# Optimization experiments

Measured on AMD Instinct MI355X. Metric: run time of the kernel, lower is better.

Reference implementation:

```python
import jax, jax.numpy as jnp
import numpy as np
from jax import lax

DIM = 128
DEPTH = 2
OUT_DIM = 256
DIM_HEAD = 64
HEADS = 8
WS = 16
INNER = DIM_HEAD * HEADS
EPS = 1e-5
SCALE = DIM_HEAD ** (-0.5)


def setup_inputs() -> dict:
    key = jax.random.key(0)
    ks = jax.random.split(key, 20)
    s = 0.02
    L = DEPTH
    inp = {
        "x": jax.random.normal(ks[0], (1, DIM, 256, 256), dtype=jnp.float32),
        "ln1_g": jnp.ones((L, DIM), dtype=jnp.float32),
        "ln1_b": jnp.zeros((L, DIM), dtype=jnp.float32),
        "wq": jax.random.normal(ks[1], (L, INNER, DIM), dtype=jnp.float32) * s,
        "wkv": jax.random.normal(ks[2], (L, 2 * INNER, DIM), dtype=jnp.float32) * s,
        "wo": jax.random.normal(ks[3], (L, DIM, INNER), dtype=jnp.float32) * s,
        "bo": jnp.zeros((L, DIM), dtype=jnp.float32),
        "ln2_g": jnp.ones((L, DIM), dtype=jnp.float32),
        "ln2_b": jnp.zeros((L, DIM), dtype=jnp.float32),
        "w_in": jax.random.normal(ks[4], (L, DIM, DIM), dtype=jnp.float32) * s,
        "b_in": jnp.zeros((L, DIM), dtype=jnp.float32),
        "w_c3": jax.random.normal(ks[5], (L, OUT_DIM, DIM, 3, 3), dtype=jnp.float32) * s,
        "b_c3": jnp.zeros((L, OUT_DIM), dtype=jnp.float32),
        "w_c1": jax.random.normal(ks[6], (L, DIM, OUT_DIM), dtype=jnp.float32) * s,
        "b_c1": jnp.zeros((L, DIM), dtype=jnp.float32),
        "w_outer": jax.random.normal(ks[7], (DIM, DIM), dtype=jnp.float32) * s,
        "b_outer": jnp.zeros((DIM,), dtype=jnp.float32),
    }
    return inp


def _layernorm(x, g, b):
    # channel-wise (dim=1) norm; note torch code uses (std + eps), not sqrt(var + eps)
    mean = jnp.mean(x, axis=1, keepdims=True)
    std = jnp.sqrt(jnp.var(x, axis=1, keepdims=True))
    return (x - mean) / (std + EPS) * g[None, :, None, None] + b[None, :, None, None]


def _conv1x1(w, x, b=None):
    y = jnp.einsum('oi,bihw->bohw', w, x)
    if b is not None:
        y = y + b[None, :, None, None]
    return y


def _to_windows(t, B, H, W):
    # [B, HEADS*DIM_HEAD, H, W] -> [B*HEADS*nx*ny, WS*WS, DIM_HEAD]
    nx, ny = H // WS, W // WS
    t = t.reshape(B, HEADS, DIM_HEAD, nx, WS, ny, WS)
    t = t.transpose(0, 1, 3, 5, 4, 6, 2)
    return t.reshape(B * HEADS * nx * ny, WS * WS, DIM_HEAD)


def _from_windows(t, B, H, W):
    nx, ny = H // WS, W // WS
    t = t.reshape(B, HEADS, nx, ny, WS, WS, DIM_HEAD)
    t = t.transpose(0, 1, 6, 2, 4, 3, 5)
    return t.reshape(B, HEADS * DIM_HEAD, H, W)


def _attention(x, wq_l, wkv_l, wo_l, bo_l):
    B, _, H, W = x.shape
    q = _conv1x1(wq_l, x)
    kv = _conv1x1(wkv_l, x)
    k, v = kv[:, :INNER], kv[:, INNER:]
    q = _to_windows(q, B, H, W)
    k = _to_windows(k, B, H, W)
    v = _to_windows(v, B, H, W)
    sim = jnp.einsum('bid,bjd->bij', q, k) * SCALE  # [nwin, 256, 256]
    attn = jax.nn.softmax(sim, axis=-1)
    out = jnp.einsum('bij,bjd->bid', attn, v)
    out = _from_windows(out, B, H, W)
    return _conv1x1(wo_l, out, bo_l)


def _feedforward(x, w_in_l, b_in_l, w_c3_l, b_c3_l, w_c1_l, b_c1_l):
    h = _conv1x1(w_in_l, x, b_in_l)
    h = lax.conv_general_dilated(h, w_c3_l, window_strides=(1, 1), padding='SAME',
                                 dimension_numbers=('NCHW', 'OIHW', 'NCHW'))
    h = h + b_c3_l[None, :, None, None]
    h = jax.nn.gelu(h, approximate=False)
    return _conv1x1(w_c1_l, h, b_c1_l)


def reference(x, ln1_g, ln1_b, wq, wkv, wo, bo, ln2_g, ln2_b,
              w_in, b_in, w_c3, b_c3, w_c1, b_c1, w_outer, b_outer):
    for l in range(DEPTH):
        xn = _layernorm(x, ln1_g[l], ln1_b[l])
        x = _attention(xn, wq[l], wkv[l], wo[l], bo[l]) + x
        xn = _layernorm(x, ln2_g[l], ln2_b[l])
        x = _feedforward(xn, w_in[l], b_in[l], w_c3[l], b_c3[l], w_c1[l], b_c1[l]) + x
    return _conv1x1(w_outer, x, b_outer) + x
```

## Files before the change

kernel.cpp:

```cpp
#include <hip/hip_runtime.h>
#include <hip/hip_bf16.h>
#include <math.h>

typedef __hip_bfloat16 bf16;
typedef float f4 __attribute__((ext_vector_type(4)));
typedef short s8 __attribute__((ext_vector_type(8)));
typedef unsigned int u2 __attribute__((ext_vector_type(2)));
typedef unsigned int u4v __attribute__((ext_vector_type(4)));

__device__ __forceinline__ void gload16(const void* g, char* l) {
  __builtin_amdgcn_global_load_lds(
      (const __attribute__((address_space(1))) unsigned int*)g,
      (__attribute__((address_space(3))) unsigned int*)l, 16, 0, 0);
}
__device__ __forceinline__ unsigned short bfr(float f) {
  bf16 h = __float2bfloat16(f);
  return *(unsigned short*)&h;
}
__device__ __forceinline__ unsigned int pk2(float a, float b) {
  return (unsigned int)bfr(a) | ((unsigned int)bfr(b) << 16);
}
__device__ __forceinline__ unsigned int pkt(float a, float b) {
  return __builtin_amdgcn_perm(__float_as_uint(b), __float_as_uint(a), 0x07060302u);
}

__global__ __launch_bounds__(256) void prep_w(
    const float* __restrict__ wq, const float* __restrict__ wkv,
    const float* __restrict__ wo, const float* __restrict__ win,
    const float* __restrict__ wc3, const float* __restrict__ wc1,
    const float* __restrict__ wout, ushort* __restrict__ cw)
{
  int i = blockIdx.x * 256 + threadIdx.x;
  float v;
  if (i < 131072) v = wq[i];
  else if (i < 393216) v = wkv[i - 131072];
  else if (i < 524288) v = wo[i - 393216];
  else if (i < 557056) v = win[i - 524288];
  else if (i < 1146880) {
    int j = i - 557056; int lyr = j / 294912; int r = j - lyr * 294912;
    int m = r / 1152; int k = r - m * 1152; int tap = k >> 7; int ic = k & 127;
    v = wc3[(((size_t)lyr * 256 + m) * 128 + ic) * 9 + tap];
  }
  else if (i < 1212416) v = wc1[i - 1146880];
  else if (i < 1228800) v = wout[i - 1212416];
  else if (i < 1230848) { cw[i] = 0; return; }
  else return;
  cw[i] = bfr(v);
}

template<bool NCHW>
__global__ __launch_bounds__(256) void ln_nhwc(
    const float* __restrict__ x, const float* __restrict__ g,
    const float* __restrict__ b, ushort* __restrict__ y)
{
  const int p = blockIdx.x * 256 + threadIdx.x;
  f4 v[32];
  float s = 0.f, s2 = 0.f;
  if constexpr (NCHW) {
#pragma unroll
    for (int i = 0; i < 32; ++i)
#pragma unroll
      for (int j = 0; j < 4; ++j) {
        float t = x[(size_t)(i * 4 + j) * 65536 + p];
        v[i][j] = t; s += t; s2 += t * t;
      }
  } else {
    const f4* base = (const f4*)(x + (size_t)p * 128);
#pragma unroll
    for (int i = 0; i < 32; ++i) {
      v[i] = base[i];
#pragma unroll
      for (int j = 0; j < 4; ++j) { s += v[i][j]; s2 += v[i][j] * v[i][j]; }
    }
  }
  float mean = s * (1.f / 128.f);
  float var = s2 * (1.f / 128.f) - mean * mean;
  var = var > 0.f ? var : 0.f;
  float inv = 1.f / (sqrtf(var) + 1e-5f);
  u2* dst = (u2*)(y + (size_t)p * 128);
#pragma unroll
  for (int i = 0; i < 32; ++i) {
    f4 gg = *(const f4*)(g + i * 4);
    f4 bb = *(const f4*)(b + i * 4);
    float f0 = (v[i][0] - mean) * inv * gg[0] + bb[0];
    float f1 = (v[i][1] - mean) * inv * gg[1] + bb[1];
    float f2 = (v[i][2] - mean) * inv * gg[2] + bb[2];
    float f3 = (v[i][3] - mean) * inv * gg[3] + bb[3];
    u2 st; st.x = pk2(f0, f1); st.y = pk2(f2, f3);
    dst[i] = st;
  }
}

template<int MODE>
__global__ __launch_bounds__(256) void gemm_nhwc(
    const ushort* __restrict__ A, const ushort* __restrict__ X,
    const float* __restrict__ bias, const float* __restrict__ res,
    void* __restrict__ out, ushort* __restrict__ out2,
    const float* __restrict__ lng, const float* __restrict__ lnb,
    ushort* __restrict__ xn, const int K, const int M)
{
  __shared__ __align__(16) char sm[32768];
  const int tid = threadIdx.x, w = tid >> 6, l = tid & 63;
  const int quad = l >> 4, l15 = l & 15;
  const int n0 = blockIdx.x * 128, m0 = blockIdx.y * 128;
  const int mh = (w & 1) * 64, nh = (w >> 1) * 64;
  const f4 fz = {0.f, 0.f, 0.f, 0.f};
  f4 acc[4][4];
#pragma unroll
  for (int a = 0; a < 4; ++a)
#pragma unroll
    for (int b2 = 0; b2 < 4; ++b2) acc[a][b2] = fz;

  const int KI = K >> 6;
  for (int kk = 0; kk < KI; ++kk) {
    if (kk) __syncthreads();
    const int k0 = kk << 6;
#pragma unroll
    for (int j = 0; j < 4; ++j) {
      int p = j * 256 + tid, r = p >> 3, c = (p & 7) ^ (r & 7);
      gload16(A + (size_t)(m0 + r) * K + k0 + c * 8, sm + (j * 256 + w * 64) * 16);
    }
#pragma unroll
    for (int j = 0; j < 4; ++j) {
      int p = j * 256 + tid, r = p >> 3, c = (p & 7) ^ (r & 7);
      gload16(X + (size_t)(n0 + r) * K + k0 + c * 8, sm + 16384 + (j * 256 + w * 64) * 16);
    }
    __syncthreads();
#pragma unroll
    for (int ks = 0; ks < 2; ++ks) {
      s8 af[4], bx[4];
#pragma unroll
      for (int mt = 0; mt < 4; ++mt) {
        int rr = mh + mt * 16 + l15;
        af[mt] = *(const s8*)(sm + rr * 128 + (((ks * 4 + quad) ^ (rr & 7)) << 4));
      }
#pragma unroll
      for (int nt = 0; nt < 4; ++nt) {
        int rr = nh + nt * 16 + l15;
        bx[nt] = *(const s8*)(sm + 16384 + rr * 128 + (((ks * 4 + quad) ^ (rr & 7)) << 4));
      }
#pragma unroll
      for (int mt = 0; mt < 4; ++mt)
#pragma unroll
        for (int nt = 0; nt < 4; ++nt)
          acc[mt][nt] = __builtin_amdgcn_mfma_f32_16x16x32_bf16(af[mt], bx[nt], acc[mt][nt], 0, 0, 0);
    }
  }

  if constexpr (MODE == 5 || MODE == 6) {
    float s1[4] = {0.f, 0.f, 0.f, 0.f}, s2[4] = {0.f, 0.f, 0.f, 0.f};
#pragma unroll
    for (int mt = 0; mt < 4; ++mt) {
      const int m = mh + mt * 16 + quad * 4;
      f4 bb = *(const f4*)(bias + m);
#pragma unroll
      for (int nt = 0; nt < 4; ++nt) {
        const int n = n0 + nh + nt * 16 + l15;
        f4 v = acc[mt][nt] + bb;
        if constexpr (MODE == 5) {
          f4 r = *(const f4*)(res + (size_t)n * 128 + m);
          v += r;
        } else {
          f4 r;
#pragma unroll
          for (int i = 0; i < 4; ++i) r[i] = res[(size_t)(m + i) * 65536 + n];
          v += r;
        }
        *(f4*)((float*)out + (size_t)n * 128 + m) = v;
        acc[mt][nt] = v;
        s1[nt] += v[0] + v[1] + v[2] + v[3];
        s2[nt] += v[0] * v[0] + v[1] * v[1] + v[2] * v[2] + v[3] * v[3];
      }
    }
    __syncthreads();
    float* pb = (float*)sm;
#pragma unroll
    for (int nt = 0; nt < 4; ++nt) {
      float a1 = s1[nt], a2 = s2[nt];
      a1 += __shfl_xor(a1, 16, 64); a1 += __shfl_xor(a1, 32, 64);
      a2 += __shfl_xor(a2, 16, 64); a2 += __shfl_xor(a2, 32, 64);
      s1[nt] = a1; s2[nt] = a2;
      if (quad == 0) {
        int pn = nh + nt * 16 + l15;
        pb[((w & 1) * 128 + pn) * 2]     = a1;
        pb[((w & 1) * 128 + pn) * 2 + 1] = a2;
      }
    }
    __syncthreads();
#pragma unroll
    for (int nt = 0; nt < 4; ++nt) {
      int pn = nh + nt * 16 + l15;
      float t1 = s1[nt] + pb[((1 - (w & 1)) * 128 + pn) * 2];
      float t2 = s2[nt] + pb[((1 - (w & 1)) * 128 + pn) * 2 + 1];
      float mean = t1 * (1.f / 128.f);
      float var = t2 * (1.f / 128.f) - mean * mean;
      var = var > 0.f ? var : 0.f;
      s1[nt] = mean;
      s2[nt] = 1.f / (sqrtf(var) + 1e-5f);
    }
#pragma unroll
    for (int mt = 0; mt < 4; ++mt) {
      const int m = mh + mt * 16 + quad * 4;
      f4 gg = *(const f4*)(lng + m);
      f4 b2 = *(const f4*)(lnb + m);
#pragma unroll
      for (int nt = 0; nt < 4; ++nt) {
        const int n = n0 + nh + nt * 16 + l15;
        f4 v = acc[mt][nt];
        float mean = s1[nt], inv = s2[nt];
        float f0 = (v[0] - mean) * inv * gg[0] + b2[0];
        float f1 = (v[1] - mean) * inv * gg[1] + b2[1];
        float f2 = (v[2] - mean) * inv * gg[2] + b2[2];
        float f3 = (v[3] - mean) * inv * gg[3] + b2[3];
        u2 st; st.x = pk2(f0, f1); st.y = pk2(f2, f3);
        *(u2*)(xn + (size_t)n * 128 + m) = st;
      }
    }
    return;
  }

#pragma unroll
  for (int mt = 0; mt < 4; ++mt) {
#pragma unroll
    for (int nt = 0; nt < 4; ++nt) {
      const int m = m0 + mh + mt * 16 + quad * 4;
      const int n = n0 + nh + nt * 16 + l15;
      f4 bb = *(const f4*)(bias + m);
      f4 v = acc[mt][nt] + bb;
      if constexpr (MODE == 0) {
        u2 st; st.x = pk2(v[0], v[1]); st.y = pk2(v[2], v[3]);
        *(u2*)((ushort*)out + (size_t)n * M + m) = st;
      } else if constexpr (MODE == 1 || MODE == 3) {
        f4 r = *(const f4*)(res + (size_t)n * M + m);
        v += r;
        *(f4*)((float*)out + (size_t)n * M + m) = v;
        if constexpr (MODE == 3) {
          u2 st; st.x = pk2(v[0], v[1]); st.y = pk2(v[2], v[3]);
          *(u2*)(out2 + (size_t)n * M + m) = st;
        }
      } else if constexpr (MODE == 4) {
        f4 r;
#pragma unroll
        for (int i = 0; i < 4; ++i) r[i] = res[(size_t)(m + i) * 65536 + n];
        v += r;
        *(f4*)((float*)out + (size_t)n * M + m) = v;
      } else {
        f4 r = *(const f4*)(res + (size_t)n * M + m);
#pragma unroll
        for (int i = 0; i < 4; ++i)
          ((float*)out)[(size_t)(m + i) * 65536 + n] = v[i] + r[i];
      }
    }
  }
}

__global__ __launch_bounds__(256) void conv3_kernel(
    const ushort* __restrict__ A, const ushort* __restrict__ X,
    const float* __restrict__ bias, ushort* __restrict__ out,
    const ushort* __restrict__ zp)
{
  __shared__ __align__(16) char sm[32768];
  const int tid = threadIdx.x, w = tid >> 6, l = tid & 63;
  const int quad = l >> 4, l15 = l & 15;
  const int n0 = blockIdx.x * 128, m0 = blockIdx.y * 128;
  const int mh = (w & 1) * 64, nh = (w >> 1) * 64;
  const f4 fz = {0.f, 0.f, 0.f, 0.f};
  f4 acc[4][4];
#pragma unroll
  for (int a = 0; a < 4; ++a)
#pragma unroll
    for (int b2 = 0; b2 < 4; ++b2) acc[a][b2] = fz;

  for (int kk = 0; kk < 18; ++kk) {
    if (kk) __syncthreads();
    const int tap = kk >> 1, ky = tap / 3, kx = tap - ky * 3;
    const int dn = (ky - 1) * 256 + (kx - 1);
    const int kseg = (kk & 1) << 6;
#pragma unroll
    for (int j = 0; j < 4; ++j) {
      int p = j * 256 + tid, r = p >> 3, c = (p & 7) ^ (r & 7);
      gload16(A + (size_t)(m0 + r) * 1152 + kk * 64 + c * 8, sm + (j * 256 + w * 64) * 16);
    }
#pragma unroll
    for (int j = 0; j < 4; ++j) {
      int p = j * 256 + tid, r = p >> 3, c = (p & 7) ^ (r & 7);
      int nl = n0 + r;
      int ys = (nl >> 8) + ky - 1, xs = (nl & 255) + kx - 1;
      const ushort* gp = ((unsigned)ys < 256u && (unsigned)xs < 256u)
                         ? X + (size_t)(nl + dn) * 128 + kseg + c * 8 : zp;
      gload16(gp, sm + 16384 + (j * 256 + w * 64) * 16);
    }
    __syncthreads();
#pragma unroll
    for (int ks = 0; ks < 2; ++ks) {
      s8 af[4], bx[4];
#pragma unroll
      for (int mt = 0; mt < 4; ++mt) {
        int rr = mh + mt * 16 + l15;
        af[mt] = *(const s8*)(sm + rr * 128 + (((ks * 4 + quad) ^ (rr & 7)) << 4));
      }
#pragma unroll
      for (int nt = 0; nt < 4; ++nt) {
        int rr = nh + nt * 16 + l15;
        bx[nt] = *(const s8*)(sm + 16384 + rr * 128 + (((ks * 4 + quad) ^ (rr & 7)) << 4));
      }
#pragma unroll
      for (int mt = 0; mt < 4; ++mt)
#pragma unroll
        for (int nt = 0; nt < 4; ++nt)
          acc[mt][nt] = __builtin_amdgcn_mfma_f32_16x16x32_bf16(af[mt], bx[nt], acc[mt][nt], 0, 0, 0);
    }
  }
#pragma unroll
  for (int mt = 0; mt < 4; ++mt) {
#pragma unroll
    for (int nt = 0; nt < 4; ++nt) {
      const int m = m0 + mh + mt * 16 + quad * 4;
      const int n = n0 + nh + nt * 16 + l15;
      f4 bb = *(const f4*)(bias + m);
      f4 v = acc[mt][nt] + bb;
      float g0 = 0.5f * v[0] * (1.f + erff(v[0] * 0.70710678118f));
      float g1 = 0.5f * v[1] * (1.f + erff(v[1] * 0.70710678118f));
      float g2 = 0.5f * v[2] * (1.f + erff(v[2] * 0.70710678118f));
      float g3 = 0.5f * v[3] * (1.f + erff(v[3] * 0.70710678118f));
      u2 st; st.x = pk2(g0, g1); st.y = pk2(g2, g3);
      *(u2*)(out + (size_t)n * 256 + m) = st;
    }
  }
}

__global__ __launch_bounds__(512) void attn_kernel(
    const ushort* __restrict__ xn, const ushort* __restrict__ wq,
    const ushort* __restrict__ wkv, ushort* __restrict__ ao)
{
  __shared__ __align__(16) char sm[147456];
  const int tid = threadIdx.x, w = tid >> 6, l = tid & 63;
  const int quad = l >> 4, l15 = l & 15;
  const int win = blockIdx.x, head = blockIdx.y;
  const int nbase = ((win >> 4) << 12) + ((win & 15) << 4);
  char* RX  = sm;
  char* RW  = sm + 65536;
  char* RK  = sm + 114688;
  char* RVT = sm;
  char* Pw  = sm + 32768 + w * 4096;
  char* RO  = RW;
  const f4 fz = {0.f, 0.f, 0.f, 0.f};

#pragma unroll
  for (int j = 0; j < 8; ++j) {
    int p = j * 512 + tid, r = p >> 4, c = (p & 15) ^ (r & 15);
    int n = nbase + ((r >> 4) << 8) + (r & 15);
    gload16(xn + (size_t)n * 128 + c * 8, RX + (j * 512 + w * 64) * 16);
  }
  {
    const ushort* wpq = wq + (size_t)head * 64 * 128;
    const ushort* wpk = wkv + (size_t)head * 64 * 128;
    const ushort* wpv = wkv + (size_t)(512 + head * 64) * 128;
#pragma unroll
    for (int j = 0; j < 2; ++j) {
      int p = j * 512 + tid, r = p >> 4, c = (p & 15) ^ (r & 15);
      gload16(wpq + (size_t)r * 128 + c * 8, RW + (j * 512 + w * 64) * 16);
    }
#pragma unroll
    for (int j = 0; j < 2; ++j) {
      int p = j * 512 + tid, r = p >> 4, c = (p & 15) ^ (r & 15);
      gload16(wpk + (size_t)r * 128 + c * 8, RW + 16384 + (j * 512 + w * 64) * 16);
    }
#pragma unroll
    for (int j = 0; j < 2; ++j) {
      int p = j * 512 + tid, r = p >> 4, c = (p & 15) ^ (r & 15);
      gload16(wpv + (size_t)r * 128 + c * 8, RW + 32768 + (j * 512 + w * 64) * 16);
    }
  }
  __syncthreads();

  s8 bq[2][2];
  {
    f4 acc[4][2];
#pragma unroll
    for (int a = 0; a < 4; ++a) { acc[a][0] = fz; acc[a][1] = fz; }
#pragma unroll
    for (int ks = 0; ks < 4; ++ks) {
      s8 af[4], bx[2];
#pragma unroll
      for (int mt = 0; mt < 4; ++mt) {
        int rr = mt * 16 + l15;
        af[mt] = *(const s8*)(RW + rr * 256 + (((ks * 4 + quad) ^ (rr & 15)) << 4));
      }
#pragma unroll
      for (int nt = 0; nt < 2; ++nt) {
        int rr = w * 32 + nt * 16 + l15;
        bx[nt] = *(const s8*)(RX + rr * 256 + (((ks * 4 + quad) ^ (rr & 15)) << 4));
      }
#pragma unroll
      for (int mt = 0; mt < 4; ++mt)
#pragma unroll
        for (int nt = 0; nt < 2; ++nt)
          acc[mt][nt] = __builtin_amdgcn_mfma_f32_16x16x32_bf16(af[mt], bx[nt], acc[mt][nt], 0, 0, 0);
    }
#pragma unroll
    for (int nt = 0; nt < 2; ++nt) {
      unsigned pd[4][2];
#pragma unroll
      for (int mt = 0; mt < 4; ++mt) {
        pd[mt][0] = pkt(acc[mt][nt][0], acc[mt][nt][1]);
        pd[mt][1] = pkt(acc[mt][nt][2], acc[mt][nt][3]);
      }
#pragma unroll
      for (int ks = 0; ks < 2; ++ks) {
        u4v t;
#pragma unroll
        for (int dj = 0; dj < 4; ++dj) {
          int srcl = l15 + (((quad & 1) * 2 + (dj >> 1)) << 4);
          unsigned va = (unsigned)__shfl((int)pd[2 * ks][dj & 1], srcl, 64);
          unsigned vb = (unsigned)__shfl((int)pd[2 * ks + 1][dj & 1], srcl, 64);
          t[dj] = (quad < 2) ? va : vb;
        }
        bq[nt][ks] = __builtin_bit_cast(s8, t);
      }
    }
  }

  {
    f4 acc[4][2];
#pragma unroll
    for (int a = 0; a < 4; ++a) { acc[a][0] = fz; acc[a][1] = fz; }
#pragma unroll
    for (int ks = 0; ks < 4; ++ks) {
      s8 af[4], bx[2];
#pragma unroll
      for (int mt = 0; mt < 4; ++mt) {
        int rr = mt * 16 + l15;
        af[mt] = *(const s8*)(RW + 16384 + rr * 256 + (((ks * 4 + quad) ^ (rr & 15)) << 4));
      }
#pragma unroll
      for (int nt = 0; nt < 2; ++nt) {
        int rr = w * 32 + nt * 16 + l15;
        bx[nt] = *(const s8*)(RX + rr * 256 + (((ks * 4 + quad) ^ (rr & 15)) << 4));
      }
#pragma unroll
      for (int mt = 0; mt < 4; ++mt)
#pragma unroll
        for (int nt = 0; nt < 2; ++nt)
          acc[mt][nt] = __builtin_amdgcn_mfma_f32_16x16x32_bf16(af[mt], bx[nt], acc[mt][nt], 0, 0, 0);
    }
#pragma unroll
    for (int mt = 0; mt < 4; ++mt)
#pragma unroll
      for (int nt = 0; nt < 2; ++nt) {
        int tok = w * 32 + nt * 16 + l15, d0 = mt * 16 + quad * 4;
        char* a = RK + tok * 128 + (((d0 >> 3) ^ (tok & 7)) << 4) + (d0 & 7) * 2;
        *(unsigned int*)a = pkt(acc[mt][nt][0], acc[mt][nt][1]);
        *(unsigned int*)(a + 4) = pkt(acc[mt][nt][2], acc[mt][nt][3]);
      }
  }

  {
    f4 acc[2][4];
#pragma unroll
    for (int a = 0; a < 2; ++a)
#pragma unroll
      for (int b2 = 0; b2 < 4; ++b2) acc[a][b2] = fz;
#pragma unroll
    for (int ks = 0; ks < 4; ++ks) {
      s8 ax[2], bw[4];
#pragma unroll
      for (int mt = 0; mt < 2; ++mt) {
        int rr = w * 32 + mt * 16 + l15;
        ax[mt] = *(const s8*)(RX + rr * 256 + (((ks * 4 + quad) ^ (rr & 15)) << 4));
      }
#pragma unroll
      for (int nt = 0; nt < 4; ++nt) {
        int rr = nt * 16 + l15;
        bw[nt] = *(const s8*)(RW + 32768 + rr * 256 + (((ks * 4 + quad) ^ (rr & 15)) << 4));
      }
#pragma unroll
      for (int mt = 0; mt < 2; ++mt)
#pragma unroll
        for (int nt = 0; nt < 4; ++nt)
          acc[mt][nt] = __builtin_amdgcn_mfma_f32_16x16x32_bf16(ax[mt], bw[nt], acc[mt][nt], 0, 0, 0);
    }
    __syncthreads();
#pragma unroll
    for (int mt = 0; mt < 2; ++mt)
#pragma unroll
      for (int nt = 0; nt < 4; ++nt) {
        int d = nt * 16 + l15, t0 = w * 32 + mt * 16 + quad * 4;
        char* a = RVT + d * 512 + (((t0 >> 3) ^ (d & 31)) << 4) + (t0 & 7) * 2;
        *(unsigned int*)a = pkt(acc[mt][nt][0], acc[mt][nt][1]);
        *(unsigned int*)(a + 4) = pkt(acc[mt][nt][2], acc[mt][nt][3]);
      }
  }
  __syncthreads();

  f4 o[4][2];
  float lsum[2] = {0.f, 0.f};
#pragma unroll
  for (int a = 0; a < 4; ++a) { o[a][0] = fz; o[a][1] = fz; }

  for (int jt = 0; jt < 4; ++jt) {
    f4 s[4][2];
#pragma unroll
    for (int a = 0; a < 4; ++a) { s[a][0] = fz; s[a][1] = fz; }
#pragma unroll
    for (int ks = 0; ks < 2; ++ks) {
      s8 af[4];
#pragma unroll
      for (int mt = 0; mt < 4; ++mt) {
        int rr = jt * 64 + mt * 16 + l15;
        af[mt] = *(const s8*)(RK + rr * 128 + (((ks * 4 + quad) ^ (rr & 7)) << 4));
      }
      __builtin_amdgcn_s_setprio(1);
#pragma unroll
      for (int mt = 0; mt < 4; ++mt)
#pragma unroll
        for (int nt = 0; nt < 2; ++nt)
          s[mt][nt] = __builtin_amdgcn_mfma_f32_16x16x32_bf16(af[mt], bq[nt][ks], s[mt][nt], 0, 0, 0);
      __builtin_amdgcn_s_setprio(0);
    }
#pragma unroll
    for (int mt = 0; mt < 4; ++mt)
#pragma unroll
      for (int nt = 0; nt < 2; ++nt) {
        float p0 = exp2f(s[mt][nt][0] * 0.18033688f);
        float p1 = exp2f(s[mt][nt][1] * 0.18033688f);
        float p2 = exp2f(s[mt][nt][2] * 0.18033688f);
        float p3 = exp2f(s[mt][nt][3] * 0.18033688f);
        lsum[nt] += p0 + p1 + p2 + p3;
        int iL = nt * 16 + l15, j0 = mt * 16 + quad * 4;
        char* a = Pw + iL * 128 + (((j0 >> 3) ^ (iL & 7)) << 4) + (j0 & 7) * 2;
        *(unsigned int*)a = pkt(p0, p1);
        *(unsigned int*)(a + 4) = pkt(p2, p3);
      }
#pragma unroll
    for (int ks = 0; ks < 2; ++ks) {
      s8 av[4], bp[2];
#pragma unroll
      for (int mt = 0; mt < 4; ++mt) {
        int d = mt * 16 + l15;
        av[mt] = *(const s8*)(RVT + d * 512 + (((jt * 8 + ks * 4 + quad) ^ (d & 31)) << 4));
      }
#pragma unroll
      for (int nt = 0; nt < 2; ++nt) {
        int iL = nt * 16 + l15;
        bp[nt] = *(const s8*)(Pw + iL * 128 + (((ks * 4 + quad) ^ (iL & 7)) << 4));
      }
      __builtin_amdgcn_s_setprio(1);
#pragma unroll
      for (int mt = 0; mt < 4; ++mt)
#pragma unroll
        for (int nt = 0; nt < 2; ++nt)
          o[mt][nt] = __builtin_amdgcn_mfma_f32_16x16x32_bf16(av[mt], bp[nt], o[mt][nt], 0, 0, 0);
      __builtin_amdgcn_s_setprio(0);
    }
  }

  float inv[2];
#pragma unroll
  for (int nt = 0; nt < 2; ++nt) {
    float v = lsum[nt];
    v += __shfl_xor(v, 16, 64);
    v += __shfl_xor(v, 32, 64);
    inv[nt] = 1.f / v;
  }
#pragma unroll
  for (int mt = 0; mt < 4; ++mt)
#pragma unroll
    for (int nt = 0; nt < 2; ++nt) {
      int i = w * 32 + nt * 16 + l15, d0 = mt * 16 + quad * 4;
      char* a = RO + i * 128 + (((d0 >> 3) ^ (i & 7)) << 4) + (d0 & 7) * 2;
      *(unsigned int*)a = pkt(o[mt][nt][0] * inv[nt], o[mt][nt][1] * inv[nt]);
      *(unsigned int*)(a + 4) = pkt(o[mt][nt][2] * inv[nt], o[mt][nt][3] * inv[nt]);
    }
  __syncthreads();
  const int tok = tid >> 1, half = tid & 1;
  const int n = nbase + ((tok >> 4) << 8) + (tok & 15);
  ushort* dst = ao + (size_t)n * 512 + head * 64 + half * 32;
#pragma unroll
  for (int c = 0; c < 4; ++c) {
    u4v v = *(const u4v*)(RO + tok * 128 + (((half * 4 + c) ^ (tok & 7)) << 4));
    *(u4v*)(dst + c * 8) = v;
  }
}

extern "C" void kernel_launch(void* const* d_in, const int* in_sizes, int n_in,
                              void* d_out, int out_size, void* d_ws, size_t ws_size,
                              hipStream_t stream)
{
  const float* x_in    = (const float*)d_in[0];
  const float* ln1_g   = (const float*)d_in[1];
  const float* ln1_b   = (const float*)d_in[2];
  const float* wq      = (const float*)d_in[3];
  const float* wkv     = (const float*)d_in[4];
  const float* wo      = (const float*)d_in[5];
  const float* bo      = (const float*)d_in[6];
  const float* ln2_g   = (const float*)d_in[7];
  const float* ln2_b   = (const float*)d_in[8];
  const float* w_in    = (const float*)d_in[9];
  const float* b_in    = (const float*)d_in[10];
  const float* w_c3    = (const float*)d_in[11];
  const float* b_c3    = (const float*)d_in[12];
  const float* w_c1    = (const float*)d_in[13];
  const float* b_c1    = (const float*)d_in[14];
  const float* w_outer = (const float*)d_in[15];
  const float* b_outer = (const float*)d_in[16];

  char* wsb = (char*)d_ws;
  ushort* CW = (ushort*)wsb;
  float*  XH = (float*)(wsb + 4194304);
  ushort* XN = (ushort*)(wsb + 37748736);
  ushort* AO = (ushort*)(wsb + 54525952);
  ushort* H  = (ushort*)(wsb + 121634816);
  ushort* G  = (ushort*)(wsb + 138412032);
  ushort* XB = (ushort*)(wsb + 171966464);

  const ushort* zp = CW + 1228800;
  dim3 b256(256);

  prep_w<<<dim3(4808), b256, 0, stream>>>(wq, wkv, wo, w_in, w_c3, w_c1, w_outer, CW);

  ln_nhwc<true><<<dim3(256), b256, 0, stream>>>(x_in, ln1_g, ln1_b, XN);
  attn_kernel<<<dim3(256, 8), dim3(512), 0, stream>>>(XN, CW, CW + 131072, AO);
  gemm_nhwc<6><<<dim3(512, 1), b256, 0, stream>>>(CW + 393216, AO, bo, x_in, XH,
      nullptr, ln2_g, ln2_b, XN, 512, 128);
  gemm_nhwc<0><<<dim3(512, 1), b256, 0, stream>>>(CW + 524288, XN, b_in, nullptr, H,
      nullptr, nullptr, nullptr, nullptr, 128, 128);
  conv3_kernel<<<dim3(512, 2), b256, 0, stream>>>(CW + 557056, H, b_c3, G, zp);
  gemm_nhwc<5><<<dim3(512, 1), b256, 0, stream>>>(CW + 1146880, G, b_c1, XH, XH,
      nullptr, ln1_g + 128, ln1_b + 128, XN, 256, 128);

  attn_kernel<<<dim3(256, 8), dim3(512), 0, stream>>>(XN, CW + 65536, CW + 262144, AO);
  gemm_nhwc<5><<<dim3(512, 1), b256, 0, stream>>>(CW + 458752, AO, bo + 128, XH, XH,
      nullptr, ln2_g + 128, ln2_b + 128, XN, 512, 128);
  gemm_nhwc<0><<<dim3(512, 1), b256, 0, stream>>>(CW + 540672, XN, b_in + 128, nullptr, H,
      nullptr, nullptr, nullptr, nullptr, 128, 128);
  conv3_kernel<<<dim3(512, 2), b256, 0, stream>>>(CW + 851968, H, b_c3 + 256, G, zp);
  gemm_nhwc<3><<<dim3(512, 1), b256, 0, stream>>>(CW + 1179648, G, b_c1 + 128, XH, XH,
      XB, nullptr, nullptr, nullptr, 256, 128);

  gemm_nhwc<2><<<dim3(512, 1), b256, 0, stream>>>(CW + 1212416, XB, b_outer, XH, d_out,
      nullptr, nullptr, nullptr, nullptr, 128, 128);
}
```

Measured before the change: 619.0 us.

## Fold 1x1 input conv into 3x3 conv weights with border bias correction

Removes the separate 1x1 projection GEMM before the 3x3 conv by multiplying w_in into the conv3 weights at prep time. The projection bias b_in becomes a per-tap term, and because the conv zero-pads the projected tensor, the epilogue subtracts the taps that fall outside the image at border rows and columns. This drops one GEMM launch and the write and read of the H intermediate per layer. It adds a weight-folding prep kernel and more epilogue arithmetic, and folding before bf16 rounding changes numerics slightly.

```diff
diff --git a/kernel.cpp b/kernel.cpp
--- a/kernel.cpp
+++ b/kernel.cpp
@@ -35,17 +35,66 @@
   if (i < 131072) v = wq[i];
   else if (i < 393216) v = wkv[i - 131072];
   else if (i < 524288) v = wo[i - 393216];
-  else if (i < 557056) v = win[i - 524288];
-  else if (i < 1146880) {
-    int j = i - 557056; int lyr = j / 294912; int r = j - lyr * 294912;
-    int m = r / 1152; int k = r - m * 1152; int tap = k >> 7; int ic = k & 127;
-    v = wc3[(((size_t)lyr * 256 + m) * 128 + ic) * 9 + tap];
-  }
+  else if (i < 1146880) return;
   else if (i < 1212416) v = wc1[i - 1146880];
   else if (i < 1228800) v = wout[i - 1212416];
   else if (i < 1230848) { cw[i] = 0; return; }
   else return;
   cw[i] = bfr(v);
+}
+
+__global__ __launch_bounds__(128) void prep_fold(
+    const float* __restrict__ wc3, const float* __restrict__ win,
+    const float* __restrict__ b_in, ushort* __restrict__ cw3out,
+    float* __restrict__ T)
+{
+  __shared__ float col[128][9];
+  __shared__ float sred[2][9];
+  const int lyr = blockIdx.x >> 8, m = blockIdx.x & 255;
+  const int tid = threadIdx.x;
+  const float* src = wc3 + (((size_t)lyr * 256 + m) * 128 + tid) * 9;
+#pragma unroll
+  for (int t = 0; t < 9; ++t) col[tid][t] = src[t];
+  float bi = b_in[lyr * 128 + tid];
+  float sb[9];
+#pragma unroll
+  for (int t = 0; t < 9; ++t) {
+    float v = col[tid][t] * bi;
+    v += __shfl_xor(v, 1, 64);  v += __shfl_xor(v, 2, 64);
+    v += __shfl_xor(v, 4, 64);  v += __shfl_xor(v, 8, 64);
+    v += __shfl_xor(v, 16, 64); v += __shfl_xor(v, 32, 64);
+    sb[t] = v;
+  }
+  if ((tid & 63) == 0) {
+#pragma unroll
+    for (int t = 0; t < 9; ++t) sred[tid >> 6][t] = sb[t];
+  }
+  __syncthreads();
+  float acc[9] = {0.f,0.f,0.f,0.f,0.f,0.f,0.f,0.f,0.f};
+  const float* wrow = win + (size_t)lyr * 16384 + tid;
+  for (int c = 0; c < 128; ++c) {
+    float wv = wrow[(size_t)c * 128];
+#pragma unroll
+    for (int t = 0; t < 9; ++t) acc[t] += col[c][t] * wv;
+  }
+  ushort* dst = cw3out + (size_t)lyr * 294912 + (size_t)m * 1152 + tid;
+#pragma unroll
+  for (int t = 0; t < 9; ++t) dst[t * 128] = bfr(acc[t]);
+  if (tid == 0) {
+    float s[9];
+#pragma unroll
+    for (int t = 0; t < 9; ++t) s[t] = sred[0][t] + sred[1][t];
+    float* Tl = T + lyr * 2304;
+    Tl[0 * 256 + m] = s[0]+s[1]+s[2]+s[3]+s[4]+s[5]+s[6]+s[7]+s[8];
+    Tl[1 * 256 + m] = s[0] + s[1] + s[2];
+    Tl[2 * 256 + m] = s[6] + s[7] + s[8];
+    Tl[3 * 256 + m] = s[0] + s[3] + s[6];
+    Tl[4 * 256 + m] = s[2] + s[5] + s[8];
+    Tl[5 * 256 + m] = s[0];
+    Tl[6 * 256 + m] = s[2];
+    Tl[7 * 256 + m] = s[6];
+    Tl[8 * 256 + m] = s[8];
+  }
 }
 
 template<bool NCHW>
@@ -257,7 +306,7 @@
 __global__ __launch_bounds__(256) void conv3_kernel(
     const ushort* __restrict__ A, const ushort* __restrict__ X,
     const float* __restrict__ bias, ushort* __restrict__ out,
-    const ushort* __restrict__ zp)
+    const ushort* __restrict__ zp, const float* __restrict__ T)
 {
   __shared__ __align__(16) char sm[32768];
   const int tid = threadIdx.x, w = tid >> 6, l = tid & 63;
@@ -311,14 +360,32 @@
           acc[mt][nt] = __builtin_amdgcn_mfma_f32_16x16x32_bf16(af[mt], bx[nt], acc[mt][nt], 0, 0, 0);
     }
   }
+  const int y = n0 >> 8;
+  const bool y0 = (y == 0), y1 = (y == 255);
+  const int xbase = (n0 & 255) + nh;
 #pragma unroll
   for (int mt = 0; mt < 4; ++mt) {
+    const int m = m0 + mh + mt * 16 + quad * 4;
+    f4 base = *(const f4*)(bias + m) + *(const f4*)(T + m);
+    f4 Lc = *(const f4*)(T + 3 * 256 + m);
+    f4 Rc = *(const f4*)(T + 4 * 256 + m);
+    if (y0) {
+      base -= *(const f4*)(T + 1 * 256 + m);
+      Lc -= *(const f4*)(T + 5 * 256 + m);
+      Rc -= *(const f4*)(T + 6 * 256 + m);
+    }
+    if (y1) {
+      base -= *(const f4*)(T + 2 * 256 + m);
+      Lc -= *(const f4*)(T + 7 * 256 + m);
+      Rc -= *(const f4*)(T + 8 * 256 + m);
+    }
 #pragma unroll
     for (int nt = 0; nt < 4; ++nt) {
-      const int m = m0 + mh + mt * 16 + quad * 4;
       const int n = n0 + nh + nt * 16 + l15;
-      f4 bb = *(const f4*)(bias + m);
-      f4 v = acc[mt][nt] + bb;
+      const int x = xbase + nt * 16 + l15;
+      float fx0 = (x == 0) ? 1.f : 0.f;
+      float fx1 = (x == 255) ? 1.f : 0.f;
+      f4 v = acc[mt][nt] + base - Lc * fx0 - Rc * fx1;
       float g0 = 0.5f * v[0] * (1.f + erff(v[0] * 0.70710678118f));
       float g1 = 0.5f * v[1] * (1.f + erff(v[1] * 0.70710678118f));
       float g2 = 0.5f * v[2] * (1.f + erff(v[2] * 0.70710678118f));
@@ -607,10 +674,10 @@
 
   char* wsb = (char*)d_ws;
   ushort* CW = (ushort*)wsb;
+  float*  TB = (float*)(wsb + 3145728);
   float*  XH = (float*)(wsb + 4194304);
   ushort* XN = (ushort*)(wsb + 37748736);
   ushort* AO = (ushort*)(wsb + 54525952);
-  ushort* H  = (ushort*)(wsb + 121634816);
   ushort* G  = (ushort*)(wsb + 138412032);
   ushort* XB = (ushort*)(wsb + 171966464);
 
@@ -618,23 +685,20 @@
   dim3 b256(256);
 
   prep_w<<<dim3(4808), b256, 0, stream>>>(wq, wkv, wo, w_in, w_c3, w_c1, w_outer, CW);
+  prep_fold<<<dim3(512), dim3(128), 0, stream>>>(w_c3, w_in, b_in, CW + 557056, TB);
 
   ln_nhwc<true><<<dim3(256), b256, 0, stream>>>(x_in, ln1_g, ln1_b, XN);
   attn_kernel<<<dim3(256, 8), dim3(512), 0, stream>>>(XN, CW, CW + 131072, AO);
   gemm_nhwc<6><<<dim3(512, 1), b256, 0, stream>>>(CW + 393216, AO, bo, x_in, XH,
       nullptr, ln2_g, ln2_b, XN, 512, 128);
-  gemm_nhwc<0><<<dim3(512, 1), b256, 0, stream>>>(CW + 524288, XN, b_in, nullptr, H,
-      nullptr, nullptr, nullptr, nullptr, 128, 128);
-  conv3_kernel<<<dim3(512, 2), b256, 0, stream>>>(CW + 557056, H, b_c3, G, zp);
+  conv3_kernel<<<dim3(512, 2), b256, 0, stream>>>(CW + 557056, XN, b_c3, G, zp, TB);
   gemm_nhwc<5><<<dim3(512, 1), b256, 0, stream>>>(CW + 1146880, G, b_c1, XH, XH,
       nullptr, ln1_g + 128, ln1_b + 128, XN, 256, 128);
 
   attn_kernel<<<dim3(256, 8), dim3(512), 0, stream>>>(XN, CW + 65536, CW + 262144, AO);
   gemm_nhwc<5><<<dim3(512, 1), b256, 0, stream>>>(CW + 458752, AO, bo + 128, XH, XH,
       nullptr, ln2_g + 128, ln2_b + 128, XN, 512, 128);
-  gemm_nhwc<0><<<dim3(512, 1), b256, 0, stream>>>(CW + 540672, XN, b_in + 128, nullptr, H,
-      nullptr, nullptr, nullptr, nullptr, 128, 128);
-  conv3_kernel<<<dim3(512, 2), b256, 0, stream>>>(CW + 851968, H, b_c3 + 256, G, zp);
+  conv3_kernel<<<dim3(512, 2), b256, 0, stream>>>(CW + 851968, XN, b_c3 + 256, G, zp, TB + 2304);
   gemm_nhwc<3><<<dim3(512, 1), b256, 0, stream>>>(CW + 1179648, G, b_c1 + 128, XH, XH,
       XB, nullptr, nullptr, nullptr, 256, 128);
 
```

Result: no change. 620.9 us (+0.3%).
